# Kernel tuning notes

Measured on AMD Instinct MI355X. Metric: run time of the kernel, lower is better.

The kernel has to match this reference:

```python
import jax, jax.numpy as jnp
import numpy as np

WS = 7
B, Dd, Hh, Wd, C, NH = 1, 28, 28, 28, 384, 12

def _rel_index(ws):
    coords = np.stack(np.meshgrid(np.arange(ws), np.arange(ws), np.arange(ws), indexing='ij'))
    cf = coords.reshape(3, -1)
    rel = (cf[:, :, None] - cf[:, None, :]).transpose(1, 2, 0) + (ws - 1)
    rel[:, :, 0] *= (2 * ws - 1) ** 2
    rel[:, :, 1] *= (2 * ws - 1)
    return rel.sum(-1)  # (ws^3, ws^3)

REL_IDX = _rel_index(WS)

def setup_inputs():
    key = jax.random.key(0)
    ks = jax.random.split(key, 8)
    L = Dd * Hh * Wd
    s = 0.02
    return {
        'skip': jax.random.normal(ks[0], (B, L, C), jnp.float32),
        'x_up': jax.random.normal(ks[1], (B, L, C), jnp.float32),
        'D': Dd, 'H': Hh, 'W': Wd,
        'ln1_g': jnp.ones((C,), jnp.float32), 'ln1_b': jnp.zeros((C,), jnp.float32),
        'kv_w': jax.random.normal(ks[2], (C, 2 * C), jnp.float32) * s,
        'kv_b': jnp.zeros((2 * C,), jnp.float32),
        'rpb': jax.random.normal(ks[3], ((2 * WS - 1) ** 3, NH), jnp.float32) * s,
        'proj_w': jax.random.normal(ks[4], (C, C), jnp.float32) * s,
        'proj_b': jnp.zeros((C,), jnp.float32),
        'ln2_g': jnp.ones((C,), jnp.float32), 'ln2_b': jnp.zeros((C,), jnp.float32),
        'mlp_w1': jax.random.normal(ks[5], (C, 4 * C), jnp.float32) * s,
        'mlp_b1': jnp.zeros((4 * C,), jnp.float32),
        'mlp_w2': jax.random.normal(ks[6], (4 * C, C), jnp.float32) * s,
        'mlp_b2': jnp.zeros((C,), jnp.float32),
    }

def _ln(x, g, b):
    m = jnp.mean(x, -1, keepdims=True)
    v = jnp.mean(jnp.square(x - m), -1, keepdims=True)
    return (x - m) * jax.lax.rsqrt(v + 1e-5) * g + b

def _win_part(x):
    b, d, h, w, c = x.shape
    x = x.reshape(b, d // WS, WS, h // WS, WS, w // WS, WS, c)
    return x.transpose(0, 1, 3, 5, 2, 4, 6, 7).reshape(-1, WS ** 3, c)

def _win_rev(x, b, d, h, w):
    c = x.shape[-1]
    x = x.reshape(b, d // WS, h // WS, w // WS, WS, WS, WS, c)
    return x.transpose(0, 1, 4, 2, 5, 3, 6, 7).reshape(b, d, h, w, c)

def reference(skip, x_up, D, H, W, ln1_g, ln1_b, kv_w, kv_b, rpb, proj_w, proj_b, ln2_g, ln2_b, mlp_w1, mlp_b1, mlp_w2, mlp_b2):
    b, L, c = skip.shape
    x = x_up + skip  # wrapper residual; shortcut of the inner block
    # inner block was built with shift_size=0 -> no cyclic shift, attn_mask unused
    sk = _win_part(_ln(skip, ln1_g, ln1_b).reshape(b, D, H, W, c))   # (nW, N, C) -> K,V source
    qx = _win_part(_ln(x_up, ln1_g, ln1_b).reshape(b, D, H, W, c))   # (nW, N, C) -> Q source
    nW, N, _ = sk.shape
    hd = c // NH
    kv = (sk @ kv_w + kv_b).reshape(nW, N, 2, NH, hd)
    k, v = kv[:, :, 0], kv[:, :, 1]                  # (nW, N, NH, hd)
    q = qx.reshape(nW, N, NH, hd) * (hd ** -0.5)     # no q projection in WindowAttention_kv
    attn = jnp.einsum('wqhd,wkhd->whqk', q, k)
    bias = rpb[REL_IDX.reshape(-1)].reshape(N, N, NH).transpose(2, 0, 1)
    attn = jax.nn.softmax(attn + bias[None], axis=-1)
    o = jnp.einsum('whqk,wkhd->wqhd', attn, v).reshape(nW, N, c)
    o = o @ proj_w + proj_b
    o = _win_rev(o, b, D, H, W).reshape(b, L, c)
    x = x + o
    h1 = jax.nn.gelu(_ln(x, ln2_g, ln2_b) @ mlp_w1 + mlp_b1)
    x = x + h1 @ mlp_w2 + mlp_b2
    return x
```

## Files before the change

### kernel.cpp

```cpp
#include <hip/hip_runtime.h>
#include <hip/hip_bf16.h>
#include <cstdint>

typedef unsigned short u16;
typedef short s16x8 __attribute__((ext_vector_type(8)));
typedef float f32x4 __attribute__((ext_vector_type(4)));

#define C_DIM 384
#define NHEAD 12
#define HD    32
#define NTOK  343
#define NWIN  64
#define LTOT  21952
#define SIDE  28

__device__ __forceinline__ float u2f(u16 u) {
    return __uint_as_float(((unsigned int)u) << 16);
}
__device__ __forceinline__ u16 f2b(float f) {
    unsigned int u = __float_as_uint(f);
    return (u16)((u + 0x7fffu + ((u >> 16) & 1u)) >> 16);
}
__device__ __forceinline__ float gelu_fast(float x) {
    float z = 0.7978845608028654f * (x + 0.044715f * x * x * x);
    return x / (1.f + __expf(-2.f * z));
}

__global__ __launch_bounds__(256) void k_wt(
    const float* __restrict__ W, u16* __restrict__ Wt, int K, int N)
{
    __shared__ float T[64][65];
    int k0 = blockIdx.x * 64, n0 = blockIdx.y * 64;
    int t = threadIdx.x;
    int c = t & 63, rg = t >> 6;
#pragma unroll
    for (int i = 0; i < 16; i++) {
        int r = rg * 16 + i;
        T[r][c] = W[(size_t)(k0 + r) * N + n0 + c];
    }
    __syncthreads();
    int k = t & 63, ng = t >> 6;
#pragma unroll
    for (int i = 0; i < 16; i++) {
        int n = ng * 16 + i;
        Wt[(size_t)(n0 + n) * K + k0 + k] = f2b(T[k][n]);
    }
}

__global__ __launch_bounds__(256) void k_lnprep(
    const float* __restrict__ skip, const float* __restrict__ xup,
    const float* __restrict__ g, const float* __restrict__ bta,
    u16* __restrict__ skW, u16* __restrict__ qW, u16* __restrict__ res)
{
    int t = blockIdx.x * 4 + (threadIdx.x >> 6);
    int lane = threadIdx.x & 63;
    const float* ps = skip + (size_t)t * C_DIM;
    const float* px = xup + (size_t)t * C_DIM;
    float vs[6], vx[6];
    float s1 = 0.f, s2 = 0.f, x1 = 0.f, x2 = 0.f;
#pragma unroll
    for (int j = 0; j < 6; j++) {
        float a = ps[lane + j * 64];
        float b = px[lane + j * 64];
        vs[j] = a; vx[j] = b;
        s1 += a; s2 += a * a; x1 += b; x2 += b * b;
    }
#pragma unroll
    for (int off = 32; off; off >>= 1) {
        s1 += __shfl_xor(s1, off);
        s2 += __shfl_xor(s2, off);
        x1 += __shfl_xor(x1, off);
        x2 += __shfl_xor(x2, off);
    }
    float ms = s1 * (1.f / 384.f), mx = x1 * (1.f / 384.f);
    float rs = rsqrtf(fmaxf(s2 * (1.f / 384.f) - ms * ms, 0.f) + 1e-5f);
    float rx = rsqrtf(fmaxf(x2 * (1.f / 384.f) - mx * mx, 0.f) + 1e-5f);
    int d = t / 784, rem = t % 784, hh = rem / 28, ww = rem % 28;
    int win = (d / 7) * 16 + (hh / 7) * 4 + (ww / 7);
    int n = (d % 7) * 49 + (hh % 7) * 7 + (ww % 7);
    size_t dst = ((size_t)(win * NTOK + n)) * C_DIM + lane;
    size_t td  = (size_t)t * C_DIM + lane;
#pragma unroll
    for (int j = 0; j < 6; j++) {
        int c = lane + j * 64;
        float gg = g[c], bb = bta[c];
        skW[dst + j * 64] = f2b((vs[j] - ms) * rs * gg + bb);
        qW[dst + j * 64]  = f2b((vx[j] - mx) * rx * gg + bb);
        res[td + j * 64]  = f2b(vs[j] + vx[j]);
    }
}

__global__ __launch_bounds__(256) void k_ln2(
    const u16* __restrict__ x2, const float* __restrict__ g,
    const float* __restrict__ bta, u16* __restrict__ lnx)
{
    int t = blockIdx.x * 4 + (threadIdx.x >> 6);
    int lane = threadIdx.x & 63;
    const u16* p = x2 + (size_t)t * C_DIM;
    float v[6];
    float s1 = 0.f, s2 = 0.f;
#pragma unroll
    for (int j = 0; j < 6; j++) {
        float a = u2f(p[lane + j * 64]);
        v[j] = a; s1 += a; s2 += a * a;
    }
#pragma unroll
    for (int off = 32; off; off >>= 1) {
        s1 += __shfl_xor(s1, off);
        s2 += __shfl_xor(s2, off);
    }
    float m = s1 * (1.f / 384.f);
    float r = rsqrtf(fmaxf(s2 * (1.f / 384.f) - m * m, 0.f) + 1e-5f);
    size_t dst = (size_t)t * C_DIM + lane;
#pragma unroll
    for (int j = 0; j < 6; j++) {
        int c = lane + j * 64;
        lnx[dst + j * 64] = f2b((v[j] - m) * r * g[c] + bta[c]);
    }
}

#define BPAD 40

__device__ __forceinline__ void gemm128(
    const u16* __restrict__ A, const u16* __restrict__ Bt, int K, int M,
    int rowBase, int colBase, int tid,
    u16 (*As)[BPAD], u16 (*Bs)[BPAD], f32x4 acc[2][8])
{
    const int sr  = tid >> 2;
    const int scg = (tid & 3) << 3;
    const int lane = tid & 63, wv = tid >> 6;
    const int m16 = lane & 15, quad = lane >> 4;

    int ra0 = min(rowBase + sr, M - 1);
    int ra1 = min(rowBase + 64 + sr, M - 1);
    const u16* pa0 = A + (size_t)ra0 * K + scg;
    const u16* pa1 = A + (size_t)ra1 * K + scg;
    const u16* pb0 = Bt + (size_t)(colBase + sr) * K + scg;
    const u16* pb1 = Bt + (size_t)(colBase + 64 + sr) * K + scg;

    uint4 a0 = *(const uint4*)pa0, a1 = *(const uint4*)pa1;
    uint4 b0 = *(const uint4*)pb0, b1 = *(const uint4*)pb1;

    for (int kk = 0; kk < K; kk += 32) {
        *(uint4*)&As[sr][scg]      = a0;
        *(uint4*)&As[64 + sr][scg] = a1;
        *(uint4*)&Bs[sr][scg]      = b0;
        *(uint4*)&Bs[64 + sr][scg] = b1;
        __syncthreads();
        if (kk + 32 < K) {
            a0 = *(const uint4*)(pa0 + kk + 32);
            a1 = *(const uint4*)(pa1 + kk + 32);
            b0 = *(const uint4*)(pb0 + kk + 32);
            b1 = *(const uint4*)(pb1 + kk + 32);
        }
        s16x8 af0 = *(const s16x8*)&As[wv * 32 + m16][quad * 8];
        s16x8 af1 = *(const s16x8*)&As[wv * 32 + 16 + m16][quad * 8];
#pragma unroll
        for (int c = 0; c < 8; c++) {
            s16x8 bf = *(const s16x8*)&Bs[c * 16 + m16][quad * 8];
            acc[0][c] = __builtin_amdgcn_mfma_f32_16x16x32_bf16(af0, bf, acc[0][c], 0, 0, 0);
            acc[1][c] = __builtin_amdgcn_mfma_f32_16x16x32_bf16(af1, bf, acc[1][c], 0, 0, 0);
        }
        __syncthreads();
    }
}

__device__ __forceinline__ void gemm64_d2(
    const u16* __restrict__ A, const u16* __restrict__ Bt, int K, int M,
    int rowBase, int colBase, int tid,
    u16 (*As)[BPAD], u16 (*Bs)[BPAD], f32x4 acc[8])
{
    const int sr  = tid >> 2;
    const int scg = (tid & 3) << 3;
    const int lane = tid & 63, wv = tid >> 6;
    const int m16 = lane & 15, quad = lane >> 4;

    int ra = min(rowBase + sr, M - 1);
    const u16* pa  = A + (size_t)ra * K + scg;
    const u16* pb0 = Bt + (size_t)(colBase + sr) * K + scg;
    const u16* pb1 = Bt + (size_t)(colBase + 64 + sr) * K + scg;

    uint4 a0  = *(const uint4*)pa;
    uint4 b00 = *(const uint4*)pb0;
    uint4 b01 = *(const uint4*)pb1;
    uint4 a1  = *(const uint4*)(pa + 32);
    uint4 b10 = *(const uint4*)(pb0 + 32);
    uint4 b11 = *(const uint4*)(pb1 + 32);

    for (int kk = 0; kk < K; kk += 64) {
        *(uint4*)&As[sr][scg]      = a0;
        *(uint4*)&Bs[sr][scg]      = b00;
        *(uint4*)&Bs[64 + sr][scg] = b01;
        __syncthreads();
        if (kk + 64 < K) {
            a0  = *(const uint4*)(pa  + kk + 64);
            b00 = *(const uint4*)(pb0 + kk + 64);
            b01 = *(const uint4*)(pb1 + kk + 64);
        }
        {
            s16x8 af = *(const s16x8*)&As[wv * 16 + m16][quad * 8];
#pragma unroll
            for (int c = 0; c < 8; c++) {
                s16x8 bf = *(const s16x8*)&Bs[c * 16 + m16][quad * 8];
                acc[c] = __builtin_amdgcn_mfma_f32_16x16x32_bf16(af, bf, acc[c], 0, 0, 0);
            }
        }
        __syncthreads();
        *(uint4*)&As[sr][scg]      = a1;
        *(uint4*)&Bs[sr][scg]      = b10;
        *(uint4*)&Bs[64 + sr][scg] = b11;
        __syncthreads();
        if (kk + 96 < K) {
            a1  = *(const uint4*)(pa  + kk + 96);
            b10 = *(const uint4*)(pb0 + kk + 96);
            b11 = *(const uint4*)(pb1 + kk + 96);
        }
        {
            s16x8 af = *(const s16x8*)&As[wv * 16 + m16][quad * 8];
#pragma unroll
            for (int c = 0; c < 8; c++) {
                s16x8 bf = *(const s16x8*)&Bs[c * 16 + m16][quad * 8];
                acc[c] = __builtin_amdgcn_mfma_f32_16x16x32_bf16(af, bf, acc[c], 0, 0, 0);
            }
        }
        __syncthreads();
    }
}

#define EPI_SETUP \
    int lane = tid & 63, wv = tid >> 6, quad = lane >> 4, n16 = lane & 15;

__global__ __launch_bounds__(256) void k_gemm_kv(
    const u16* __restrict__ A, const u16* __restrict__ Wt, const float* __restrict__ bias,
    u16* __restrict__ Kb, u16* __restrict__ Vb)
{
    __shared__ __align__(16) u16 As[128][BPAD];
    __shared__ __align__(16) u16 Bs[128][BPAD];
    f32x4 acc[2][8] = {};
    int tid = threadIdx.x;
    int rowBase = blockIdx.x * 128, colBase = blockIdx.y * 128;
    gemm128(A, Wt, 384, LTOT, rowBase, colBase, tid, As, Bs, acc);
    EPI_SETUP
#pragma unroll
    for (int c = 0; c < 8; c++) {
        int col = colBase + c * 16 + n16;
        float bcol = bias[col];
        int isv = col >= 384;
        int remc = col - (isv ? 384 : 0);
        int hh = remc >> 5, dd = remc & 31;
#pragma unroll
        for (int rt = 0; rt < 2; rt++)
#pragma unroll
        for (int reg = 0; reg < 4; reg++) {
            int r = rowBase + wv * 32 + rt * 16 + quad * 4 + reg;
            if (r < LTOT) {
                int w = r / NTOK, nn = r % NTOK;
                size_t dst = ((size_t)((w * NHEAD + hh) * NTOK + nn)) * HD + dd;
                (isv ? Vb : Kb)[dst] = f2b(acc[rt][c][reg] + bcol);
            }
        }
    }
}

__global__ __launch_bounds__(256) void k_gemm_proj(
    const u16* __restrict__ A, const u16* __restrict__ Wt, const float* __restrict__ bias,
    const u16* __restrict__ res, u16* __restrict__ x2)
{
    __shared__ __align__(16) u16 As[64][BPAD];
    __shared__ __align__(16) u16 Bs[128][BPAD];
    f32x4 acc[8] = {};
    int tid = threadIdx.x;
    int rowBase = blockIdx.x * 64, colBase = blockIdx.y * 128;
    gemm64_d2(A, Wt, 384, LTOT, rowBase, colBase, tid, As, Bs, acc);
    EPI_SETUP
#pragma unroll
    for (int c = 0; c < 8; c++) {
        int col = colBase + c * 16 + n16;
        float bcol = bias[col];
#pragma unroll
        for (int reg = 0; reg < 4; reg++) {
            int r = rowBase + wv * 16 + quad * 4 + reg;
            if (r < LTOT) {
                size_t idx = (size_t)r * C_DIM + col;
                x2[idx] = f2b(acc[c][reg] + bcol + u2f(res[idx]));
            }
        }
    }
}

__global__ __launch_bounds__(256) void k_gemm_mlp1(
    const u16* __restrict__ A, const u16* __restrict__ Wt, const float* __restrict__ bias,
    u16* __restrict__ h1c, int rowOfs)
{
    __shared__ __align__(16) u16 As[128][BPAD];
    __shared__ __align__(16) u16 Bs[128][BPAD];
    f32x4 acc[2][8] = {};
    int tid = threadIdx.x;
    int rowBase = rowOfs + blockIdx.x * 128, colBase = blockIdx.y * 128;
    gemm128(A, Wt, 384, LTOT, rowBase, colBase, tid, As, Bs, acc);
    EPI_SETUP
#pragma unroll
    for (int c = 0; c < 8; c++) {
        int col = colBase + c * 16 + n16;
        float bcol = bias[col];
#pragma unroll
        for (int rt = 0; rt < 2; rt++)
#pragma unroll
        for (int reg = 0; reg < 4; reg++) {
            int r = rowBase + wv * 32 + rt * 16 + quad * 4 + reg;
            if (r < LTOT) {
                size_t rl = (size_t)(r - rowOfs);
                h1c[rl * 1536 + col] = f2b(gelu_fast(acc[rt][c][reg] + bcol));
            }
        }
    }
}

__global__ __launch_bounds__(256) void k_gemm_mlp2(
    const u16* __restrict__ A, const u16* __restrict__ Wt, const float* __restrict__ bias,
    const u16* __restrict__ x2, float* __restrict__ out, int rowOfs, int chunkRows)
{
    __shared__ __align__(16) u16 As[64][BPAD];
    __shared__ __align__(16) u16 Bs[128][BPAD];
    f32x4 acc[8] = {};
    int tid = threadIdx.x;
    int rowBase = blockIdx.x * 64, colBase = blockIdx.y * 128;
    gemm64_d2(A, Wt, 1536, chunkRows, rowBase, colBase, tid, As, Bs, acc);
    EPI_SETUP
#pragma unroll
    for (int c = 0; c < 8; c++) {
        int col = colBase + c * 16 + n16;
        float bcol = bias[col];
#pragma unroll
        for (int reg = 0; reg < 4; reg++) {
            int rl = rowBase + wv * 16 + quad * 4 + reg;
            int rg = rowOfs + rl;
            if (rl < chunkRows && rg < LTOT) {
                size_t idx = (size_t)rg * C_DIM + col;
                out[idx] = acc[c][reg] + bcol + u2f(x2[idx]);
            }
        }
    }
}

#define KP 40
#define VP 360

__global__ __launch_bounds__(256, 2) void k_attn(
    const u16* __restrict__ qW, const u16* __restrict__ Kb, const u16* __restrict__ Vb,
    const float* __restrict__ rpb, u16* __restrict__ oT)
{
    __shared__ __align__(16) u16 Ks[352 * KP];
    __shared__ __align__(16) u16 Vt[32 * VP];
    __shared__ __align__(16) u16 rp16[2208];
    __shared__ __align__(16) u16 code[352];
    __shared__ __align__(16) u16 Pb[4 * 16 * KP];

    const int h = blockIdx.x, w = blockIdx.y, half = blockIdx.z;
    const int tid = threadIdx.x;
    const int lane = tid & 63, wv = tid >> 6;
    const int m16 = lane & 15, quad = lane >> 4;
    const size_t base = ((size_t)(w * NHEAD + h)) * NTOK * HD;

    for (int t = tid; t < 1408; t += 256) {
        int r = t >> 2, c = (t & 3) << 3;
        uint4 u = make_uint4(0, 0, 0, 0);
        if (r < NTOK) u = *(const uint4*)(Kb + base + r * HD + c);
        *(uint4*)&Ks[r * KP + c] = u;
    }
    for (int t = tid; t < 1408; t += 256) {
        int dg = t / 352, n = t - dg * 352;
        uint4 u = make_uint4(0, 0, 0, 0);
        if (n < NTOK) u = *(const uint4*)(Vb + base + n * HD + dg * 8);
        int d0 = dg * 8;
        Vt[(d0 + 0) * VP + n] = (u16)(u.x & 0xffff);
        Vt[(d0 + 1) * VP + n] = (u16)(u.x >> 16);
        Vt[(d0 + 2) * VP + n] = (u16)(u.y & 0xffff);
        Vt[(d0 + 3) * VP + n] = (u16)(u.y >> 16);
        Vt[(d0 + 4) * VP + n] = (u16)(u.z & 0xffff);
        Vt[(d0 + 5) * VP + n] = (u16)(u.z >> 16);
        Vt[(d0 + 6) * VP + n] = (u16)(u.w & 0xffff);
        Vt[(d0 + 7) * VP + n] = (u16)(u.w >> 16);
    }
    for (int t = tid; t < 2208; t += 256)
        rp16[t] = (t < 2197) ? f2b(rpb[t * NHEAD + h]) : (u16)0;
    for (int t = tid; t < 352; t += 256) {
        int z = t / 49, rem = t % 49, y = rem / 7, x = rem % 7;
        code[t] = (t < NTOK) ? (u16)(z * 169 + y * 13 + x) : (u16)1098;
    }
    __syncthreads();

    const float scale = 0.17677669529663687f;
    u16* myP = Pb + wv * 16 * KP;

    for (int qt = half * 11 + wv; qt < half * 11 + 11; qt += 4) {
        int qbase = qt * 16;
        int qrow = min(qbase + m16, NTOK - 1);
        s16x8 qf = *(const s16x8*)(qW + ((size_t)(w * NTOK + qrow)) * C_DIM
                                       + h * HD + quad * 8);
        int qcv[4];
#pragma unroll
        for (int i = 0; i < 4; i++) qcv[i] = code[qbase + quad * 4 + i];

        f32x4 S0[11], S1[11];
        float mx[4] = {-1e30f, -1e30f, -1e30f, -1e30f};

#pragma unroll
        for (int ks = 0; ks < 11; ks++) {
            int kbase = ks * 32;
            int kt0 = kbase + m16, kt1 = kt0 + 16;
            s16x8 kf0 = *(const s16x8*)&Ks[kt0 * KP + quad * 8];
            s16x8 kf1 = *(const s16x8*)&Ks[kt1 * KP + quad * 8];
            f32x4 z = {0.f, 0.f, 0.f, 0.f};
            f32x4 sA = __builtin_amdgcn_mfma_f32_16x16x32_bf16(qf, kf0, z, 0, 0, 0);
            f32x4 sB = __builtin_amdgcn_mfma_f32_16x16x32_bf16(qf, kf1, z, 0, 0, 0);
            int kc0 = code[kt0], kc1 = code[kt1];
            bool k1ok = (ks < 10) || (kt1 < NTOK);
#pragma unroll
            for (int i = 0; i < 4; i++) {
                float b0 = u2f(rp16[qcv[i] - kc0 + 1098]);
                float b1 = u2f(rp16[qcv[i] - kc1 + 1098]);
                float sa = fmaf(sA[i], scale, b0);
                float sb = k1ok ? fmaf(sB[i], scale, b1) : -1e30f;
                S0[ks][i] = sa;
                S1[ks][i] = sb;
                mx[i] = fmaxf(mx[i], fmaxf(sa, sb));
            }
        }
#pragma unroll
        for (int i = 0; i < 4; i++) {
            float v = mx[i];
            v = fmaxf(v, __shfl_xor(v, 1));
            v = fmaxf(v, __shfl_xor(v, 2));
            v = fmaxf(v, __shfl_xor(v, 4));
            v = fmaxf(v, __shfl_xor(v, 8));
            mx[i] = v;
        }

        f32x4 O0 = {}, O1 = {};
        float l[4] = {};
#pragma unroll
        for (int ks = 0; ks < 11; ks++) {
            int kbase = ks * 32;
#pragma unroll
            for (int i = 0; i < 4; i++) {
                float pa = __expf(S0[ks][i] - mx[i]);
                float pb = __expf(S1[ks][i] - mx[i]);
                l[i] += pa + pb;
                int prow = quad * 4 + i;
                myP[prow * KP + m16]      = f2b(pa);
                myP[prow * KP + 16 + m16] = f2b(pb);
            }
            s16x8 pf  = *(const s16x8*)&myP[m16 * KP + quad * 8];
            s16x8 vf0 = *(const s16x8*)&Vt[m16 * VP + kbase + quad * 8];
            s16x8 vf1 = *(const s16x8*)&Vt[(16 + m16) * VP + kbase + quad * 8];
            O0 = __builtin_amdgcn_mfma_f32_16x16x32_bf16(pf, vf0, O0, 0, 0, 0);
            O1 = __builtin_amdgcn_mfma_f32_16x16x32_bf16(pf, vf1, O1, 0, 0, 0);
        }
#pragma unroll
        for (int i = 0; i < 4; i++) {
            float v = l[i];
            v += __shfl_xor(v, 1);
            v += __shfl_xor(v, 2);
            v += __shfl_xor(v, 4);
            v += __shfl_xor(v, 8);
            l[i] = v;
        }

        int wd = w >> 4, wh = (w >> 2) & 3, wwi = w & 3;
#pragma unroll
        for (int i = 0; i < 4; i++) {
            int q = qbase + quad * 4 + i;
            if (q < NTOK) {
                float rl = 1.f / l[i];
                int qz = q / 49, qrem = q % 49, qy = qrem / 7, qx = qrem % 7;
                size_t tok = ((size_t)(wd * 7 + qz) * SIDE + (wh * 7 + qy)) * SIDE
                             + (wwi * 7 + qx);
                u16* op = oT + tok * C_DIM + h * HD;
                op[m16]      = f2b(O0[i] * rl);
                op[16 + m16] = f2b(O1[i] * rl);
            }
        }
    }
}

extern "C" void kernel_launch(void* const* d_in, const int* in_sizes, int n_in,
                              void* d_out, int out_size, void* d_ws, size_t ws_size,
                              hipStream_t stream)
{
    const float* skip = (const float*)d_in[0];
    const float* xup  = (const float*)d_in[1];
    const float* ln1g = (const float*)d_in[5];
    const float* ln1b = (const float*)d_in[6];
    const float* kvw  = (const float*)d_in[7];
    const float* kvb  = (const float*)d_in[8];
    const float* rpb  = (const float*)d_in[9];
    const float* pw   = (const float*)d_in[10];
    const float* pb   = (const float*)d_in[11];
    const float* ln2g = (const float*)d_in[12];
    const float* ln2b = (const float*)d_in[13];
    const float* w1   = (const float*)d_in[14];
    const float* b1   = (const float*)d_in[15];
    const float* w2   = (const float*)d_in[16];
    const float* b2   = (const float*)d_in[17];
    float* out = (float*)d_out;

    char* ws = (char*)d_ws;
    const size_t BUFB = (size_t)LTOT * C_DIM * 2;
    const size_t WTB  = 589824 + 294912 + 1179648 + 1179648;
    u16* skW = (u16*)(ws);
    u16* qW  = (u16*)(ws + BUFB);
    u16* Kb  = (u16*)(ws + 2 * BUFB);
    u16* Vb  = (u16*)(ws + 3 * BUFB);
    u16* oT  = (u16*)(ws);
    u16* x2  = (u16*)(ws + BUFB);
    u16* lnx = (u16*)(ws + 2 * BUFB);
    char* wt = ws + 4 * BUFB;
    u16* kvWt = (u16*)(wt);
    u16* pWt  = (u16*)(wt + 589824);
    u16* w1t  = (u16*)(wt + 589824 + 294912);
    u16* w2t  = (u16*)(wt + 589824 + 294912 + 1179648);
    u16* res  = (u16*)d_out;

    const size_t used = 4 * BUFB + WTB;
    const size_t blkBytes = 128 * 1536 * 2;
    size_t tailCap = (ws_size > used) ? (ws_size - used) / blkBytes : 0;
    int chunkBlocks;
    u16* h1c;
    if (tailCap >= 43) {
        chunkBlocks = tailCap < 172 ? (int)tailCap : 172;
        h1c = (u16*)(ws + used);
    } else {
        chunkBlocks = 42;
        h1c = (u16*)(ws + 3 * BUFB);
    }

    k_wt<<<dim3(6, 12), 256, 0, stream>>>(kvw, kvWt, 384, 768);
    k_wt<<<dim3(6, 6),  256, 0, stream>>>(pw,  pWt,  384, 384);
    k_wt<<<dim3(6, 24), 256, 0, stream>>>(w1,  w1t,  384, 1536);
    k_wt<<<dim3(24, 6), 256, 0, stream>>>(w2,  w2t,  1536, 384);

    k_lnprep<<<LTOT / 4, 256, 0, stream>>>(skip, xup, ln1g, ln1b, skW, qW, res);
    k_gemm_kv<<<dim3(172, 6), 256, 0, stream>>>(skW, kvWt, kvb, Kb, Vb);
    k_attn<<<dim3(NHEAD, NWIN, 2), 256, 0, stream>>>(qW, Kb, Vb, rpb, oT);
    k_gemm_proj<<<dim3(343, 3), 256, 0, stream>>>(oT, pWt, pb, res, x2);
    k_ln2<<<LTOT / 4, 256, 0, stream>>>(x2, ln2g, ln2b, lnx);
    for (int b0 = 0; b0 < 172; b0 += chunkBlocks) {
        int nb = (172 - b0) < chunkBlocks ? (172 - b0) : chunkBlocks;
        int rowOfs = b0 * 128;
        int chunkRows = nb * 128;
        if (rowOfs + chunkRows > LTOT) chunkRows = LTOT - rowOfs;
        int nb64 = (chunkRows + 63) / 64;
        k_gemm_mlp1<<<dim3(nb, 12), 256, 0, stream>>>(lnx, w1t, b1, h1c, rowOfs);
        k_gemm_mlp2<<<dim3(nb64, 3), 256, 0, stream>>>(h1c, w2t, b2, x2, out, rowOfs, chunkRows);
    }
}
```

Measured before the change: 450.4 us.

## Use exp2 hardware ops, packed bf16 stores, and merged attention halves

Several changes land at once. The attention kernel now runs one 512-thread block per (head, window) instead of two 256-thread halves, so K/V staging is no longer duplicated. The scale and relative-position bias are pre-multiplied by log2(e) so raw v_exp_f32 can be used, and P is stored as packed bf16 pairs in a permuted column order. The V transpose writes packed 32-bit words. The MLP1 epilogue writes packed bf16 pairs with permuted columns, w2 is transposed with a matching k-permutation to compensate, and GELU uses exp2 with an rcp intrinsic. The risks are correctness of the permutation bookkeeping, slightly lower exp/rcp accuracy, and the occupancy effects of 512-thread blocks.

New measurement: 493.9 us. +9.6%, slower.

```diff
diff --git a/kernel.cpp b/kernel.cpp
--- a/kernel.cpp
+++ b/kernel.cpp
@@ -4,6 +4,7 @@
 
 typedef unsigned short u16;
 typedef short s16x8 __attribute__((ext_vector_type(8)));
+typedef short s16x4 __attribute__((ext_vector_type(4)));
 typedef float f32x4 __attribute__((ext_vector_type(4)));
 
 #define C_DIM 384
@@ -21,9 +22,19 @@
     unsigned int u = __float_as_uint(f);
     return (u16)((u + 0x7fffu + ((u >> 16) & 1u)) >> 16);
 }
+__device__ __forceinline__ float exp2_hw(float x) {
+    float r;
+    asm("v_exp_f32 %0, %1" : "=v"(r) : "v"(x));
+    return r;
+}
+__device__ __forceinline__ unsigned int pk_bf16(float lo, float hi) {
+    unsigned int r;
+    asm("v_cvt_pk_bf16_f32 %0, %1, %2" : "=v"(r) : "v"(lo), "v"(hi));
+    return r;
+}
 __device__ __forceinline__ float gelu_fast(float x) {
-    float z = 0.7978845608028654f * (x + 0.044715f * x * x * x);
-    return x / (1.f + __expf(-2.f * z));
+    float e = exp2_hw(-2.3022083f * (x + 0.044715f * x * x * x));
+    return x * __builtin_amdgcn_rcpf(1.f + e);
 }
 
 __global__ __launch_bounds__(256) void k_wt(
@@ -44,6 +55,30 @@
     for (int i = 0; i < 16; i++) {
         int n = ng * 16 + i;
         Wt[(size_t)(n0 + n) * K + k0 + k] = f2b(T[k][n]);
+    }
+}
+
+__global__ __launch_bounds__(256) void k_wt_pi(
+    const float* __restrict__ W, u16* __restrict__ Wt, int K, int N)
+{
+    __shared__ float T[64][65];
+    int k0 = blockIdx.x * 64, n0 = blockIdx.y * 64;
+    int t = threadIdx.x;
+    int c = t & 63, rg = t >> 6;
+#pragma unroll
+    for (int i = 0; i < 16; i++) {
+        int r = rg * 16 + i;
+        T[r][c] = W[(size_t)(k0 + r) * N + n0 + c];
+    }
+    __syncthreads();
+    int k = t & 63, ng = t >> 6;
+    int kg = k0 + k;
+    int j = kg & 127, ct = j >> 4, nn = j & 15;
+    int kp = (kg & ~127) | ((ct >> 1) << 5) | (nn << 1) | (ct & 1);
+#pragma unroll
+    for (int i = 0; i < 16; i++) {
+        int n = ng * 16 + i;
+        Wt[(size_t)(n0 + n) * K + kp] = f2b(T[k][n]);
     }
 }
 
@@ -300,9 +335,11 @@
     gemm128(A, Wt, 384, LTOT, rowBase, colBase, tid, As, Bs, acc);
     EPI_SETUP
 #pragma unroll
-    for (int c = 0; c < 8; c++) {
-        int col = colBase + c * 16 + n16;
-        float bcol = bias[col];
+    for (int p = 0; p < 4; p++) {
+        int col0 = colBase + p * 32 + n16;
+        int col1 = col0 + 16;
+        float bc0 = bias[col0], bc1 = bias[col1];
+        int dcol = colBase + p * 32 + 2 * n16;
 #pragma unroll
         for (int rt = 0; rt < 2; rt++)
 #pragma unroll
@@ -310,7 +347,9 @@
             int r = rowBase + wv * 32 + rt * 16 + quad * 4 + reg;
             if (r < LTOT) {
                 size_t rl = (size_t)(r - rowOfs);
-                h1c[rl * 1536 + col] = f2b(gelu_fast(acc[rt][c][reg] + bcol));
+                float v0 = gelu_fast(acc[rt][2 * p][reg] + bc0);
+                float v1 = gelu_fast(acc[rt][2 * p + 1][reg] + bc1);
+                *(unsigned int*)&h1c[rl * 1536 + dcol] = pk_bf16(v0, v1);
             }
         }
     }
@@ -343,57 +382,69 @@
     }
 }
 
-#define KP 40
-#define VP 360
-
-__global__ __launch_bounds__(256, 2) void k_attn(
+#define KP  40
+#define VP  360
+#define PBS 36
+
+__global__ __launch_bounds__(512, 4) void k_attn(
     const u16* __restrict__ qW, const u16* __restrict__ Kb, const u16* __restrict__ Vb,
     const float* __restrict__ rpb, u16* __restrict__ oT)
 {
     __shared__ __align__(16) u16 Ks[352 * KP];
     __shared__ __align__(16) u16 Vt[32 * VP];
-    __shared__ __align__(16) u16 rp16[2208];
+    __shared__ __align__(16) u16 rp16[2200];
     __shared__ __align__(16) u16 code[352];
-    __shared__ __align__(16) u16 Pb[4 * 16 * KP];
-
-    const int h = blockIdx.x, w = blockIdx.y, half = blockIdx.z;
+    __shared__ __align__(16) u16 Pb[8 * 16 * PBS];
+
+    const int h = blockIdx.x, w = blockIdx.y;
     const int tid = threadIdx.x;
     const int lane = tid & 63, wv = tid >> 6;
     const int m16 = lane & 15, quad = lane >> 4;
     const size_t base = ((size_t)(w * NHEAD + h)) * NTOK * HD;
 
-    for (int t = tid; t < 1408; t += 256) {
+    for (int t = tid; t < 1408; t += 512) {
         int r = t >> 2, c = (t & 3) << 3;
         uint4 u = make_uint4(0, 0, 0, 0);
         if (r < NTOK) u = *(const uint4*)(Kb + base + r * HD + c);
         *(uint4*)&Ks[r * KP + c] = u;
     }
-    for (int t = tid; t < 1408; t += 256) {
-        int dg = t / 352, n = t - dg * 352;
-        uint4 u = make_uint4(0, 0, 0, 0);
-        if (n < NTOK) u = *(const uint4*)(Vb + base + n * HD + dg * 8);
-        int d0 = dg * 8;
-        Vt[(d0 + 0) * VP + n] = (u16)(u.x & 0xffff);
-        Vt[(d0 + 1) * VP + n] = (u16)(u.x >> 16);
-        Vt[(d0 + 2) * VP + n] = (u16)(u.y & 0xffff);
-        Vt[(d0 + 3) * VP + n] = (u16)(u.y >> 16);
-        Vt[(d0 + 4) * VP + n] = (u16)(u.z & 0xffff);
-        Vt[(d0 + 5) * VP + n] = (u16)(u.z >> 16);
-        Vt[(d0 + 6) * VP + n] = (u16)(u.w & 0xffff);
-        Vt[(d0 + 7) * VP + n] = (u16)(u.w >> 16);
-    }
-    for (int t = tid; t < 2208; t += 256)
-        rp16[t] = (t < 2197) ? f2b(rpb[t * NHEAD + h]) : (u16)0;
-    for (int t = tid; t < 352; t += 256) {
+    for (int t = tid; t < 704; t += 512) {
+        int dg = t / 176, rem = t - dg * 176;
+        int kb = rem >> 4, j = rem & 15;
+        int n0 = kb * 32 + j, n1 = n0 + 16;
+        uint4 uA = make_uint4(0, 0, 0, 0), uB = make_uint4(0, 0, 0, 0);
+        if (n0 < NTOK) uA = *(const uint4*)(Vb + base + n0 * HD + dg * 8);
+        if (n1 < NTOK) uB = *(const uint4*)(Vb + base + n1 * HD + dg * 8);
+        int d0 = dg * 8, colu = kb * 32 + 2 * j;
+        unsigned int pk0 = (uA.x & 0xffffu) | (uB.x << 16);
+        unsigned int pk1 = (uA.x >> 16)     | (uB.x & 0xffff0000u);
+        unsigned int pk2 = (uA.y & 0xffffu) | (uB.y << 16);
+        unsigned int pk3 = (uA.y >> 16)     | (uB.y & 0xffff0000u);
+        unsigned int pk4 = (uA.z & 0xffffu) | (uB.z << 16);
+        unsigned int pk5 = (uA.z >> 16)     | (uB.z & 0xffff0000u);
+        unsigned int pk6 = (uA.w & 0xffffu) | (uB.w << 16);
+        unsigned int pk7 = (uA.w >> 16)     | (uB.w & 0xffff0000u);
+        *(unsigned int*)&Vt[(d0 + 0) * VP + colu] = pk0;
+        *(unsigned int*)&Vt[(d0 + 1) * VP + colu] = pk1;
+        *(unsigned int*)&Vt[(d0 + 2) * VP + colu] = pk2;
+        *(unsigned int*)&Vt[(d0 + 3) * VP + colu] = pk3;
+        *(unsigned int*)&Vt[(d0 + 4) * VP + colu] = pk4;
+        *(unsigned int*)&Vt[(d0 + 5) * VP + colu] = pk5;
+        *(unsigned int*)&Vt[(d0 + 6) * VP + colu] = pk6;
+        *(unsigned int*)&Vt[(d0 + 7) * VP + colu] = pk7;
+    }
+    for (int t = tid; t < 2200; t += 512)
+        rp16[t] = (t < 2197) ? f2b(rpb[t * NHEAD + h] * 1.4426950408889634f) : (u16)0;
+    for (int t = tid; t < 352; t += 512) {
         int z = t / 49, rem = t % 49, y = rem / 7, x = rem % 7;
         code[t] = (t < NTOK) ? (u16)(z * 169 + y * 13 + x) : (u16)1098;
     }
     __syncthreads();
 
-    const float scale = 0.17677669529663687f;
-    u16* myP = Pb + wv * 16 * KP;
-
-    for (int qt = half * 11 + wv; qt < half * 11 + 11; qt += 4) {
+    const float scale = 0.2550348772f;
+    u16* myP = Pb + wv * 16 * PBS;
+
+    for (int qt = wv; qt < 22; qt += 8) {
         int qbase = qt * 16;
         int qrow = min(qbase + m16, NTOK - 1);
         s16x8 qf = *(const s16x8*)(qW + ((size_t)(w * NTOK + qrow)) * C_DIM
@@ -444,14 +495,14 @@
             int kbase = ks * 32;
 #pragma unroll
             for (int i = 0; i < 4; i++) {
-                float pa = __expf(S0[ks][i] - mx[i]);
-                float pb = __expf(S1[ks][i] - mx[i]);
+                float pa = exp2_hw(S0[ks][i] - mx[i]);
+                float pb = exp2_hw(S1[ks][i] - mx[i]);
                 l[i] += pa + pb;
-                int prow = quad * 4 + i;
-                myP[prow * KP + m16]      = f2b(pa);
-                myP[prow * KP + 16 + m16] = f2b(pb);
-            }
-            s16x8 pf  = *(const s16x8*)&myP[m16 * KP + quad * 8];
+                *(unsigned int*)&myP[(quad * 4 + i) * PBS + 2 * m16] = pk_bf16(pa, pb);
+            }
+            s16x4 plo = *(const s16x4*)&myP[m16 * PBS + quad * 8];
+            s16x4 phi = *(const s16x4*)&myP[m16 * PBS + quad * 8 + 4];
+            s16x8 pf  = __builtin_shufflevector(plo, phi, 0, 1, 2, 3, 4, 5, 6, 7);
             s16x8 vf0 = *(const s16x8*)&Vt[m16 * VP + kbase + quad * 8];
             s16x8 vf1 = *(const s16x8*)&Vt[(16 + m16) * VP + kbase + quad * 8];
             O0 = __builtin_amdgcn_mfma_f32_16x16x32_bf16(pf, vf0, O0, 0, 0, 0);
@@ -472,7 +523,7 @@
         for (int i = 0; i < 4; i++) {
             int q = qbase + quad * 4 + i;
             if (q < NTOK) {
-                float rl = 1.f / l[i];
+                float rl = __builtin_amdgcn_rcpf(l[i]);
                 int qz = q / 49, qrem = q % 49, qy = qrem / 7, qx = qrem % 7;
                 size_t tok = ((size_t)(wd * 7 + qz) * SIDE + (wh * 7 + qy)) * SIDE
                              + (wwi * 7 + qx);
@@ -538,11 +589,11 @@
     k_wt<<<dim3(6, 12), 256, 0, stream>>>(kvw, kvWt, 384, 768);
     k_wt<<<dim3(6, 6),  256, 0, stream>>>(pw,  pWt,  384, 384);
     k_wt<<<dim3(6, 24), 256, 0, stream>>>(w1,  w1t,  384, 1536);
-    k_wt<<<dim3(24, 6), 256, 0, stream>>>(w2,  w2t,  1536, 384);
+    k_wt_pi<<<dim3(24, 6), 256, 0, stream>>>(w2, w2t, 1536, 384);
 
     k_lnprep<<<LTOT / 4, 256, 0, stream>>>(skip, xup, ln1g, ln1b, skW, qW, res);
     k_gemm_kv<<<dim3(172, 6), 256, 0, stream>>>(skW, kvWt, kvb, Kb, Vb);
-    k_attn<<<dim3(NHEAD, NWIN, 2), 256, 0, stream>>>(qW, Kb, Vb, rpb, oT);
+    k_attn<<<dim3(NHEAD, NWIN), 512, 0, stream>>>(qW, Kb, Vb, rpb, oT);
     k_gemm_proj<<<dim3(343, 3), 256, 0, stream>>>(oT, pWt, pb, res, x2);
     k_ln2<<<LTOT / 4, 256, 0, stream>>>(x2, ln2g, ln2b, lnx);
     for (int b0 = 0; b0 < 172; b0 += chunkBlocks) {
```
